# Kernel tuning notes

Hardware: AMD Instinct MI355X
Metric: run time of the kernel (lower is better)

Reference implementation:

```python
import jax, jax.numpy as jnp
import numpy as np

N, D, H, C, E = 16384, 768, 768, 2, 20

def setup_inputs() -> dict:
    key = jax.random.key(0)
    k1, k2, k3, k4, k5, k6 = jax.random.split(key, 6)
    return {
        "embeddings": jax.random.normal(k1, (N, D), dtype=jnp.float32),
        "component_idx": jax.random.randint(k2, (N,), 0, E, dtype=jnp.int64),
        "W1": jax.random.normal(k3, (E, D, H), dtype=jnp.float32) * (1.0 / np.sqrt(D)),
        "b1": jnp.zeros((E, H), dtype=jnp.float32),
        "W2": jax.random.normal(k4, (E, H, C), dtype=jnp.float32) * (1.0 / np.sqrt(H)),
        "b2": jnp.zeros((E, C), dtype=jnp.float32),
    }

def reference(embeddings, component_idx, W1, b1, W2, b2):
    # Each token n goes through expert component_idx[n]:
    #   y = relu(x @ W1[e] + b1[e]) @ W2[e] + b2[e]
    # The torch module's mask/cat/argsort reassembly is mathematically a
    # per-token select of its own expert's output at the original position.
    # Dense-expert formulation (standard jax MoE fallback), then gather.
    h = jax.nn.relu(jnp.einsum('nd,edh->enh', embeddings, W1) + b1[:, None, :])  # [E,N,H]
    y = jnp.einsum('enh,ehc->enc', h, W2) + b2[:, None, :]                        # [E,N,C]
    n_idx = jnp.arange(embeddings.shape[0])
    return y[component_idx, n_idx]  # [N,C]
```

## Files before the change

### kernel.cpp

```cpp
#include <hip/hip_runtime.h>

#define N_D 768
#define N_H 768
#define N_C 2
#define N_E 20
#define MT 128
#define NT 128
#define BK 32
#define KT (N_D / BK)
#define MAX_TILES 160
#define NCOL (N_H / NT)
#define ROWB (N_D * 2)
#define W1BLKS (N_E * (N_D / 64) * (N_H / 64))

typedef __attribute__((ext_vector_type(8))) short short8;
typedef __attribute__((ext_vector_type(4))) float f32x4;

__device__ __forceinline__ unsigned short f2bf(float f) {
  unsigned u = __builtin_bit_cast(unsigned, f);
  u += 0x7FFFu + ((u >> 16) & 1u);
  return (unsigned short)(u >> 16);
}

#define GLD_LDS16(gp, lp)                                                        \
  __builtin_amdgcn_global_load_lds(                                              \
      (const __attribute__((address_space(1))) void*)(gp),                       \
      (__attribute__((address_space(3))) void*)(lp), 16, 0, 0)


__global__ __launch_bounds__(256) void k_prep(const float* __restrict__ W1,
                                              unsigned short* __restrict__ W1t,
                                              const int* __restrict__ cidx,
                                              int* __restrict__ counts, int n,
                                              int hb) {
  __shared__ float tile[64][65];
  __shared__ int lc[N_E];
  if ((int)blockIdx.x < W1BLKS) {
    int bid = blockIdx.x;
    int e = bid / 144;
    int rem = bid - e * 144;
    int h0 = (rem % 12) * 64, d0 = (rem / 12) * 64;
    const float* src = W1 + (size_t)e * N_D * N_H;
    unsigned short* dst = W1t + (size_t)e * N_H * N_D;
    int tx = threadIdx.x & 15, ty = threadIdx.x >> 4;
#pragma unroll
    for (int s = 0; s < 4; ++s) {
      int d = s * 16 + ty;
      float4 v = *(const float4*)&src[(size_t)(d0 + d) * N_H + h0 + tx * 4];
      tile[d][tx * 4 + 0] = v.x;
      tile[d][tx * 4 + 1] = v.y;
      tile[d][tx * 4 + 2] = v.z;
      tile[d][tx * 4 + 3] = v.w;
    }
    __syncthreads();
    int px = threadIdx.x & 7, py = threadIdx.x >> 3;
#pragma unroll
    for (int s = 0; s < 2; ++s) {
      int h = s * 32 + py;
      short8 v;
#pragma unroll
      for (int j = 0; j < 8; ++j)
        v[j] = (short)f2bf(tile[px * 8 + j][h]);
      *(short8*)&dst[(size_t)(h0 + h) * N_D + d0 + px * 8] = v;
    }
  } else {
    int b = blockIdx.x - W1BLKS;
    if (threadIdx.x < N_E) lc[threadIdx.x] = 0;
    __syncthreads();
    for (int i = b * 256 + threadIdx.x; i < n; i += hb * 256) {
      int e = cidx[i];
      e = e < 0 ? 0 : (e >= N_E ? N_E - 1 : e);
      atomicAdd(&lc[e], 1);
    }
    __syncthreads();
    if (threadIdx.x < N_E) atomicAdd(&counts[threadIdx.x], lc[threadIdx.x]);
  }
}


__global__ void k_scan(const int* __restrict__ counts, int* __restrict__ offsets,
                       int* __restrict__ cursor, int* __restrict__ tiles,
                       int* __restrict__ numTiles) {
  int lane = threadIdx.x;
  int c = (lane < N_E) ? counts[lane] : 0;
  int nt = (c + MT - 1) / MT;
  int cs = c, ts = nt;
#pragma unroll
  for (int s = 1; s < 32; s <<= 1) {
    int t1 = __shfl_up(cs, s, 64);
    int t2 = __shfl_up(ts, s, 64);
    if (lane >= s) {
      cs += t1;
      ts += t2;
    }
  }
  int coff = cs - c;
  int tbase = ts - nt;
  if (lane < N_E) {
    offsets[lane] = coff;
    cursor[lane] = coff;
    for (int m = 0; m < nt; ++m) {
      int t = tbase + m;
      if (t < MAX_TILES) tiles[t] = (lane << 8) | m;
    }
  }
  if (lane == N_E - 1) *numTiles = ts > MAX_TILES ? MAX_TILES : ts;
}


#define SG_TOK 64

__global__ __launch_bounds__(256) void k_scatter_gather(
    const int* __restrict__ cidx, int* __restrict__ cursor,
    int* __restrict__ sorted, const float* __restrict__ emb,
    unsigned short* __restrict__ Xg, int n) {
  __shared__ int lc[N_E];
  __shared__ int lbase[N_E];
  __shared__ int pos_s[SG_TOK];
  const int tid = threadIdx.x;
  const int nb = (n + SG_TOK - 1) / SG_TOK;
  if ((int)blockIdx.x >= nb) {
    ushort4 z = {0, 0, 0, 0};
    ushort4* dst = (ushort4*)(Xg + (size_t)n * N_D);
    for (int k = tid; k < MT * N_D / 4; k += 256) dst[k] = z;
    return;
  }
  const int base_tok = blockIdx.x * SG_TOK;
  if (tid < N_E) lc[tid] = 0;
  __syncthreads();
  const int i = base_tok + tid;
  int e = 0, p = 0;
  if (tid < SG_TOK && i < n) {
    e = cidx[i];
    e = e < 0 ? 0 : (e >= N_E ? N_E - 1 : e);
    p = atomicAdd(&lc[e], 1);
  }
  __syncthreads();
  if (tid < N_E) lbase[tid] = atomicAdd(&cursor[tid], lc[tid]);
  __syncthreads();
  if (tid < SG_TOK) {
    if (i < n) {
      int pos = lbase[e] + p;
      sorted[pos] = i;
      pos_s[tid] = pos;
    } else {
      pos_s[tid] = -1;
    }
  }
  __syncthreads();
  const int wid = tid >> 6, lane = tid & 63;
  int nrows = n - base_tok;
  if (nrows > SG_TOK) nrows = SG_TOK;
  for (int rr = wid; rr < nrows; rr += 4) {
    const float4* s = (const float4*)(emb + (size_t)(base_tok + rr) * N_D);
    ushort4* d = (ushort4*)(Xg + (size_t)pos_s[rr] * N_D);
#pragma unroll
    for (int p2 = 0; p2 < 3; ++p2) {
      float4 v = s[lane + p2 * 64];
      ushort4 o;
      o.x = f2bf(v.x);
      o.y = f2bf(v.y);
      o.z = f2bf(v.z);
      o.w = f2bf(v.w);
      d[lane + p2 * 64] = o;
    }
  }
}


__global__ __launch_bounds__(256, 4) void k_gemm(
    const unsigned short* __restrict__ Xg, const unsigned short* __restrict__ W1t,
    const float* __restrict__ b1, const float* __restrict__ W2,
    const float* __restrict__ b2, const int* __restrict__ sorted,
    const int* __restrict__ counts, const int* __restrict__ offsets,
    const int* __restrict__ tiles, const int* __restrict__ numTiles,
    float* __restrict__ out) {
  const int nactive = *numTiles * NCOL;
  const int lin = (int)blockIdx.y * NCOL + (int)blockIdx.x;
  if (lin >= nactive) return;
  const int q = nactive >> 3, r = nactive & 7;
  const int c = lin & 7, ii = lin >> 3;
  const int wgid = (c < r ? c * (q + 1) : r * (q + 1) + (c - r) * q) + ii;
  const int tileIdx = wgid / NCOL;
  const int n0 = (wgid - tileIdx * NCOL) * NT;

  const int tv = tiles[tileIdx];
  const int e = tv >> 8;
  const int m0 = (tv & 255) * MT;
  const int off = offsets[e];
  const int cnt_rel = counts[e] - m0;

  __shared__ unsigned short lA[2][MT * BK];
  __shared__ unsigned short lB[2][NT * BK];

  const int tid = threadIdx.x;
  const int wid = tid >> 6, lane = tid & 63;
  const int wm = (wid >> 1) * 64, wn = (wid & 1) * 64;
  const int quad = lane >> 4, lm = lane & 15;

  const int R0 = wid * 32 + lm;
  const char* agp = (const char*)Xg + (size_t)(off + m0 + R0) * ROWB + quad * 16;
  const char* bgp = (const char*)W1t + (size_t)e * N_H * ROWB +
                    (size_t)(n0 + R0) * ROWB + quad * 16;
  unsigned short* lap[2] = {&lA[0][(wid * 32) * BK], &lA[1][(wid * 32) * BK]};
  unsigned short* lbp[2] = {&lB[0][(wid * 32) * BK], &lB[1][(wid * 32) * BK]};

#define ISSUE_BATCH(kk, b)                                                       \
  do {                                                                           \
    const char* a_ = agp + (kk)*64;                                              \
    const char* b_ = bgp + (kk)*64;                                              \
    GLD_LDS16(a_, lap[b]);                                                       \
    GLD_LDS16(a_ + 16 * ROWB, lap[b] + 16 * BK);                                 \
    GLD_LDS16(b_, lbp[b]);                                                       \
    GLD_LDS16(b_ + 16 * ROWB, lbp[b] + 16 * BK);                                 \
  } while (0)

  f32x4 acc[4][4] = {};

  ISSUE_BATCH(0, 0);
  ISSUE_BATCH(1, 1);

  const int fa = quad * 128 + lm * 8;

  for (int kt = 0; kt < KT; ++kt) {
    const int cur = kt & 1;
    asm volatile("s_waitcnt vmcnt(4)\n\ts_barrier" ::: "memory");
    short8 af[4], bfr[4];
    for (int i = 0; i < 4; ++i)
      af[i] = *(const short8*)&lA[cur][((wm >> 4) + i) * 512 + fa];
    for (int j = 0; j < 4; ++j)
      bfr[j] = *(const short8*)&lB[cur][((wn >> 4) + j) * 512 + fa];
    asm volatile("s_waitcnt lgkmcnt(0)\n\ts_barrier" ::: "memory");
    int kk = kt + 2;
    if (kk >= KT) kk -= KT;
    ISSUE_BATCH(kk, cur);
    for (int i = 0; i < 4; ++i)
      for (int j = 0; j < 4; ++j)
        acc[i][j] =
            __builtin_amdgcn_mfma_f32_16x16x32_bf16(af[i], bfr[j], acc[i][j], 0, 0, 0);
  }

  float y0[4][4], y1[4][4];
  for (int i = 0; i < 4; ++i)
    for (int r2 = 0; r2 < 4; ++r2) y0[i][r2] = y1[i][r2] = 0.f;

  for (int j = 0; j < 4; ++j) {
    int col = n0 + wn + j * 16 + lm;
    float bias = b1[e * N_H + col];
    float2 w2 = *(const float2*)&W2[((size_t)e * N_H + col) * N_C];
    for (int i = 0; i < 4; ++i) {
      f32x4 a = acc[i][j];
      for (int r2 = 0; r2 < 4; ++r2) {
        float h = a[r2] + bias;
        h = h > 0.f ? h : 0.f;
        y0[i][r2] += h * w2.x;
        y1[i][r2] += h * w2.y;
      }
    }
  }
  for (int s = 1; s < 16; s <<= 1) {
    for (int i = 0; i < 4; ++i)
      for (int r2 = 0; r2 < 4; ++r2) {
        y0[i][r2] += __shfl_xor(y0[i][r2], s, 64);
        y1[i][r2] += __shfl_xor(y1[i][r2], s, 64);
      }
  }
  if (lm == 0) {
    const bool add_bias = (n0 == 0) && (wn == 0);
    float bb0 = add_bias ? b2[e * N_C + 0] : 0.f;
    float bb1 = add_bias ? b2[e * N_C + 1] : 0.f;
    for (int i = 0; i < 4; ++i) {
      for (int r2 = 0; r2 < 4; ++r2) {
        int mrel = wm + i * 16 + quad * 4 + r2;
        if (mrel < cnt_rel) {
          int token = sorted[off + m0 + mrel];
          atomicAdd(&out[(size_t)token * N_C + 0], y0[i][r2] + bb0);
          atomicAdd(&out[(size_t)token * N_C + 1], y1[i][r2] + bb1);
        }
      }
    }
  }
}


extern "C" void kernel_launch(void* const* d_in, const int* in_sizes, int n_in,
                              void* d_out, int out_size, void* d_ws, size_t ws_size,
                              hipStream_t stream) {
  const float* emb = (const float*)d_in[0];
  const int* cidx = (const int*)d_in[1];
  const float* W1 = (const float*)d_in[2];
  const float* b1 = (const float*)d_in[3];
  const float* W2 = (const float*)d_in[4];
  const float* b2 = (const float*)d_in[5];
  float* out = (float*)d_out;
  const int n = in_sizes[1];

  char* ws = (char*)d_ws;
  int* counts = (int*)ws;
  int* offsets = (int*)(ws + 128);
  int* cursor = (int*)(ws + 256);
  int* numTiles = (int*)(ws + 384);
  int* tiles = (int*)(ws + 512);
  int* sorted = (int*)(ws + 2048);
  size_t sorted_bytes = ((size_t)n * 4 + 255) & ~(size_t)255;
  unsigned short* Xg = (unsigned short*)(ws + 2048 + sorted_bytes);
  int pcap = n + MT;
  unsigned short* W1t = Xg + (size_t)pcap * N_D;

  hipMemsetAsync(d_ws, 0, 2048, stream);
  hipMemsetAsync(d_out, 0, (size_t)out_size * sizeof(float), stream);
  int hb = (n + 255) / 256;
  k_prep<<<W1BLKS + hb, 256, 0, stream>>>(W1, W1t, cidx, counts, n, hb);
  k_scan<<<1, 64, 0, stream>>>(counts, offsets, cursor, tiles, numTiles);
  int nb64 = (n + SG_TOK - 1) / SG_TOK;
  k_scatter_gather<<<nb64 + 1, 256, 0, stream>>>(cidx, cursor, sorted, emb, Xg, n);
  k_gemm<<<dim3(NCOL, MAX_TILES), 256, 0, stream>>>(
      Xg, W1t, b1, W2, b2, sorted, counts, offsets, tiles, numTiles, out);
}
```

Before: 221.8 us.

## Fold memsets into prep kernel, use per-block count partials, retune launch bounds

Both hipMemsetAsync calls are removed. The histogram blocks in k_prep now write per-block count partials, which k_scan sums, so the workspace no longer needs zeroing. Those same histogram blocks also zero the output buffer. Separately, the scatter/gather kernel moves to 512-thread blocks, and the GEMM's launch-bounds occupancy hint drops from 4 to 2, allowing more registers per thread at the cost of fewer resident waves.

```diff
diff --git a/kernel.cpp b/kernel.cpp
--- a/kernel.cpp
+++ b/kernel.cpp
@@ -12,6 +12,7 @@
 #define NCOL (N_H / NT)
 #define ROWB (N_D * 2)
 #define W1BLKS (N_E * (N_D / 64) * (N_H / 64))
+#define HB 64
 
 typedef __attribute__((ext_vector_type(8))) short short8;
 typedef __attribute__((ext_vector_type(4))) float f32x4;
@@ -31,8 +32,8 @@
 __global__ __launch_bounds__(256) void k_prep(const float* __restrict__ W1,
                                               unsigned short* __restrict__ W1t,
                                               const int* __restrict__ cidx,
-                                              int* __restrict__ counts, int n,
-                                              int hb) {
+                                              int* __restrict__ partials,
+                                              float* __restrict__ out, int n) {
   __shared__ float tile[64][65];
   __shared__ int lc[N_E];
   if ((int)blockIdx.x < W1BLKS) {
@@ -65,24 +66,30 @@
     }
   } else {
     int b = blockIdx.x - W1BLKS;
-    if (threadIdx.x < N_E) lc[threadIdx.x] = 0;
+    int tid = threadIdx.x;
+    if (tid < N_E) lc[tid] = 0;
     __syncthreads();
-    for (int i = b * 256 + threadIdx.x; i < n; i += hb * 256) {
+    for (int i = b * 256 + tid; i < n; i += HB * 256) {
       int e = cidx[i];
       e = e < 0 ? 0 : (e >= N_E ? N_E - 1 : e);
       atomicAdd(&lc[e], 1);
     }
     __syncthreads();
-    if (threadIdx.x < N_E) atomicAdd(&counts[threadIdx.x], lc[threadIdx.x]);
-  }
-}
-
-
-__global__ void k_scan(const int* __restrict__ counts, int* __restrict__ offsets,
-                       int* __restrict__ cursor, int* __restrict__ tiles,
-                       int* __restrict__ numTiles) {
+    if (tid < N_E) partials[b * 32 + tid] = lc[tid];
+    for (int idx = b * 256 + tid; idx < N_C * n; idx += HB * 256) out[idx] = 0.f;
+  }
+}
+
+
+__global__ void k_scan(const int* __restrict__ partials, int* __restrict__ counts,
+                       int* __restrict__ offsets, int* __restrict__ cursor,
+                       int* __restrict__ tiles, int* __restrict__ numTiles) {
   int lane = threadIdx.x;
-  int c = (lane < N_E) ? counts[lane] : 0;
+  int c = 0;
+  if (lane < N_E) {
+#pragma unroll
+    for (int b = 0; b < HB; ++b) c += partials[b * 32 + lane];
+  }
   int nt = (c + MT - 1) / MT;
   int cs = c, ts = nt;
 #pragma unroll
@@ -97,6 +104,7 @@
   int coff = cs - c;
   int tbase = ts - nt;
   if (lane < N_E) {
+    counts[lane] = c;
     offsets[lane] = coff;
     cursor[lane] = coff;
     for (int m = 0; m < nt; ++m) {
@@ -110,7 +118,7 @@
 
 #define SG_TOK 64
 
-__global__ __launch_bounds__(256) void k_scatter_gather(
+__global__ __launch_bounds__(512) void k_scatter_gather(
     const int* __restrict__ cidx, int* __restrict__ cursor,
     int* __restrict__ sorted, const float* __restrict__ emb,
     unsigned short* __restrict__ Xg, int n) {
@@ -122,7 +130,7 @@
   if ((int)blockIdx.x >= nb) {
     ushort4 z = {0, 0, 0, 0};
     ushort4* dst = (ushort4*)(Xg + (size_t)n * N_D);
-    for (int k = tid; k < MT * N_D / 4; k += 256) dst[k] = z;
+    for (int k = tid; k < MT * N_D / 4; k += 512) dst[k] = z;
     return;
   }
   const int base_tok = blockIdx.x * SG_TOK;
@@ -151,7 +159,7 @@
   const int wid = tid >> 6, lane = tid & 63;
   int nrows = n - base_tok;
   if (nrows > SG_TOK) nrows = SG_TOK;
-  for (int rr = wid; rr < nrows; rr += 4) {
+  for (int rr = wid; rr < nrows; rr += 8) {
     const float4* s = (const float4*)(emb + (size_t)(base_tok + rr) * N_D);
     ushort4* d = (ushort4*)(Xg + (size_t)pos_s[rr] * N_D);
 #pragma unroll
@@ -168,7 +176,7 @@
 }
 
 
-__global__ __launch_bounds__(256, 4) void k_gemm(
+__global__ __launch_bounds__(256, 2) void k_gemm(
     const unsigned short* __restrict__ Xg, const unsigned short* __restrict__ W1t,
     const float* __restrict__ b1, const float* __restrict__ W2,
     const float* __restrict__ b2, const int* __restrict__ sorted,
@@ -301,19 +309,17 @@
   int* cursor = (int*)(ws + 256);
   int* numTiles = (int*)(ws + 384);
   int* tiles = (int*)(ws + 512);
-  int* sorted = (int*)(ws + 2048);
+  int* partials = (int*)(ws + 2048);
+  int* sorted = (int*)(ws + 2048 + HB * 32 * 4);
   size_t sorted_bytes = ((size_t)n * 4 + 255) & ~(size_t)255;
-  unsigned short* Xg = (unsigned short*)(ws + 2048 + sorted_bytes);
+  unsigned short* Xg = (unsigned short*)(ws + 2048 + HB * 32 * 4 + sorted_bytes);
   int pcap = n + MT;
   unsigned short* W1t = Xg + (size_t)pcap * N_D;
 
-  hipMemsetAsync(d_ws, 0, 2048, stream);
-  hipMemsetAsync(d_out, 0, (size_t)out_size * sizeof(float), stream);
-  int hb = (n + 255) / 256;
-  k_prep<<<W1BLKS + hb, 256, 0, stream>>>(W1, W1t, cidx, counts, n, hb);
-  k_scan<<<1, 64, 0, stream>>>(counts, offsets, cursor, tiles, numTiles);
+  k_prep<<<W1BLKS + HB, 256, 0, stream>>>(W1, W1t, cidx, partials, out, n);
+  k_scan<<<1, 64, 0, stream>>>(partials, counts, offsets, cursor, tiles, numTiles);
   int nb64 = (n + SG_TOK - 1) / SG_TOK;
-  k_scatter_gather<<<nb64 + 1, 256, 0, stream>>>(cidx, cursor, sorted, emb, Xg, n);
+  k_scatter_gather<<<nb64 + 1, 512, 0, stream>>>(cidx, cursor, sorted, emb, Xg, n);
   k_gemm<<<dim3(NCOL, MAX_TILES), 256, 0, stream>>>(
       Xg, W1t, b1, W2, b2, sorted, counts, offsets, tiles, numTiles, out);
 }
```

Result: faster. 207.3 us (-6.5%).

## Merge histogram and scan into one kernel, fuse W1 transpose with scatter-gather

Applied to the files above, without the earlier changes.

Expert counting and the prefix scan now run in a single one-block kernel, which also removes both memsets: counts are written directly and the output zeroing moves into the padding block of the mid kernel. The W1 bf16 transpose blocks are folded into the scatter-gather launch with an XCD-aware block mapping, so the weight conversion overlaps with the embedding gather. This goes from five stream operations to three. The gemm launch bound drops from 4 to 2 waves per SIMD, allowing more registers per thread. The cost is a serial single-block histogram over all 16K tokens.

```diff
diff --git a/kernel.cpp b/kernel.cpp
--- a/kernel.cpp
+++ b/kernel.cpp
@@ -12,6 +12,7 @@
 #define NCOL (N_H / NT)
 #define ROWB (N_D * 2)
 #define W1BLKS (N_E * (N_D / 64) * (N_H / 64))
+#define SG_TOK 64
 
 typedef __attribute__((ext_vector_type(8))) short short8;
 typedef __attribute__((ext_vector_type(4))) float f32x4;
@@ -28,21 +29,90 @@
       (__attribute__((address_space(3))) void*)(lp), 16, 0, 0)
 
 
-__global__ __launch_bounds__(256) void k_prep(const float* __restrict__ W1,
-                                              unsigned short* __restrict__ W1t,
-                                              const int* __restrict__ cidx,
-                                              int* __restrict__ counts, int n,
-                                              int hb) {
+__global__ __launch_bounds__(256) void k_front(const int* __restrict__ cidx,
+                                               int* __restrict__ counts,
+                                               int* __restrict__ offsets,
+                                               int* __restrict__ cursor,
+                                               int* __restrict__ tiles,
+                                               int* __restrict__ numTiles, int n) {
+  __shared__ int lc[4][N_E];
+  __shared__ int tot[N_E];
+  const int tid = threadIdx.x;
+  const int w = tid >> 6;
+  for (int k = tid; k < 4 * N_E; k += 256) ((int*)lc)[k] = 0;
+  __syncthreads();
+  const int4* c4 = (const int4*)cidx;
+  const int nv = n >> 2;
+  for (int i = tid; i < nv; i += 256) {
+    int4 v = c4[i];
+    int e0 = v.x < 0 ? 0 : (v.x >= N_E ? N_E - 1 : v.x);
+    int e1 = v.y < 0 ? 0 : (v.y >= N_E ? N_E - 1 : v.y);
+    int e2 = v.z < 0 ? 0 : (v.z >= N_E ? N_E - 1 : v.z);
+    int e3 = v.w < 0 ? 0 : (v.w >= N_E ? N_E - 1 : v.w);
+    atomicAdd(&lc[w][e0], 1);
+    atomicAdd(&lc[w][e1], 1);
+    atomicAdd(&lc[w][e2], 1);
+    atomicAdd(&lc[w][e3], 1);
+  }
+  for (int i = (nv << 2) + tid; i < n; i += 256) {
+    int e = cidx[i];
+    e = e < 0 ? 0 : (e >= N_E ? N_E - 1 : e);
+    atomicAdd(&lc[w][e], 1);
+  }
+  __syncthreads();
+  if (tid < N_E) tot[tid] = lc[0][tid] + lc[1][tid] + lc[2][tid] + lc[3][tid];
+  __syncthreads();
+  if (tid < 64) {
+    int lane = tid;
+    int c = (lane < N_E) ? tot[lane] : 0;
+    int nt = (c + MT - 1) / MT;
+    int cs = c, ts = nt;
+#pragma unroll
+    for (int s = 1; s < 32; s <<= 1) {
+      int t1 = __shfl_up(cs, s, 64);
+      int t2 = __shfl_up(ts, s, 64);
+      if (lane >= s) {
+        cs += t1;
+        ts += t2;
+      }
+    }
+    int coff = cs - c;
+    int tbase = ts - nt;
+    if (lane < N_E) {
+      counts[lane] = c;
+      offsets[lane] = coff;
+      cursor[lane] = coff;
+      for (int m = 0; m < nt; ++m) {
+        int t = tbase + m;
+        if (t < MAX_TILES) tiles[t] = (lane << 8) | m;
+      }
+    }
+    if (lane == N_E - 1) *numTiles = ts > MAX_TILES ? MAX_TILES : ts;
+  }
+}
+
+
+__global__ __launch_bounds__(256) void k_mid(
+    const int* __restrict__ cidx, int* __restrict__ cursor,
+    int* __restrict__ sorted, const float* __restrict__ emb,
+    unsigned short* __restrict__ Xg, const float* __restrict__ W1,
+    unsigned short* __restrict__ W1t, float* __restrict__ out, int n, int nbsg) {
   __shared__ float tile[64][65];
   __shared__ int lc[N_E];
-  if ((int)blockIdx.x < W1BLKS) {
-    int bid = blockIdx.x;
-    int e = bid / 144;
-    int rem = bid - e * 144;
+  __shared__ int lbase[N_E];
+  __shared__ int pos_s[SG_TOK];
+  const int tid = threadIdx.x;
+
+  if ((int)blockIdx.x >= nbsg) {
+    int w1i = blockIdx.x - nbsg;
+    int xcd = w1i & 7, ii = w1i >> 3;
+    int wgid = xcd * (W1BLKS / 8) + ii;
+    int e = wgid / 144;
+    int rem = wgid - e * 144;
     int h0 = (rem % 12) * 64, d0 = (rem / 12) * 64;
     const float* src = W1 + (size_t)e * N_D * N_H;
     unsigned short* dst = W1t + (size_t)e * N_H * N_D;
-    int tx = threadIdx.x & 15, ty = threadIdx.x >> 4;
+    int tx = tid & 15, ty = tid >> 4;
 #pragma unroll
     for (int s = 0; s < 4; ++s) {
       int d = s * 16 + ty;
@@ -53,7 +123,7 @@
       tile[d][tx * 4 + 3] = v.w;
     }
     __syncthreads();
-    int px = threadIdx.x & 7, py = threadIdx.x >> 3;
+    int px = tid & 7, py = tid >> 3;
 #pragma unroll
     for (int s = 0; s < 2; ++s) {
       int h = s * 32 + py;
@@ -63,66 +133,17 @@
         v[j] = (short)f2bf(tile[px * 8 + j][h]);
       *(short8*)&dst[(size_t)(h0 + h) * N_D + d0 + px * 8] = v;
     }
-  } else {
-    int b = blockIdx.x - W1BLKS;
-    if (threadIdx.x < N_E) lc[threadIdx.x] = 0;
-    __syncthreads();
-    for (int i = b * 256 + threadIdx.x; i < n; i += hb * 256) {
-      int e = cidx[i];
-      e = e < 0 ? 0 : (e >= N_E ? N_E - 1 : e);
-      atomicAdd(&lc[e], 1);
-    }
-    __syncthreads();
-    if (threadIdx.x < N_E) atomicAdd(&counts[threadIdx.x], lc[threadIdx.x]);
-  }
-}
-
-
-__global__ void k_scan(const int* __restrict__ counts, int* __restrict__ offsets,
-                       int* __restrict__ cursor, int* __restrict__ tiles,
-                       int* __restrict__ numTiles) {
-  int lane = threadIdx.x;
-  int c = (lane < N_E) ? counts[lane] : 0;
-  int nt = (c + MT - 1) / MT;
-  int cs = c, ts = nt;
-#pragma unroll
-  for (int s = 1; s < 32; s <<= 1) {
-    int t1 = __shfl_up(cs, s, 64);
-    int t2 = __shfl_up(ts, s, 64);
-    if (lane >= s) {
-      cs += t1;
-      ts += t2;
-    }
-  }
-  int coff = cs - c;
-  int tbase = ts - nt;
-  if (lane < N_E) {
-    offsets[lane] = coff;
-    cursor[lane] = coff;
-    for (int m = 0; m < nt; ++m) {
-      int t = tbase + m;
-      if (t < MAX_TILES) tiles[t] = (lane << 8) | m;
-    }
-  }
-  if (lane == N_E - 1) *numTiles = ts > MAX_TILES ? MAX_TILES : ts;
-}
-
-
-#define SG_TOK 64
-
-__global__ __launch_bounds__(256) void k_scatter_gather(
-    const int* __restrict__ cidx, int* __restrict__ cursor,
-    int* __restrict__ sorted, const float* __restrict__ emb,
-    unsigned short* __restrict__ Xg, int n) {
-  __shared__ int lc[N_E];
-  __shared__ int lbase[N_E];
-  __shared__ int pos_s[SG_TOK];
-  const int tid = threadIdx.x;
+    return;
+  }
+
   const int nb = (n + SG_TOK - 1) / SG_TOK;
   if ((int)blockIdx.x >= nb) {
     ushort4 z = {0, 0, 0, 0};
     ushort4* dst = (ushort4*)(Xg + (size_t)n * N_D);
     for (int k = tid; k < MT * N_D / 4; k += 256) dst[k] = z;
+    float4 zf = {0.f, 0.f, 0.f, 0.f};
+    float4* of = (float4*)out;
+    for (int k = tid; k < N_C * n / 4; k += 256) of[k] = zf;
     return;
   }
   const int base_tok = blockIdx.x * SG_TOK;
@@ -168,7 +189,7 @@
 }
 
 
-__global__ __launch_bounds__(256, 4) void k_gemm(
+__global__ __launch_bounds__(256, 2) void k_gemm(
     const unsigned short* __restrict__ Xg, const unsigned short* __restrict__ W1t,
     const float* __restrict__ b1, const float* __restrict__ W2,
     const float* __restrict__ b2, const int* __restrict__ sorted,
@@ -307,13 +328,10 @@
   int pcap = n + MT;
   unsigned short* W1t = Xg + (size_t)pcap * N_D;
 
-  hipMemsetAsync(d_ws, 0, 2048, stream);
-  hipMemsetAsync(d_out, 0, (size_t)out_size * sizeof(float), stream);
-  int hb = (n + 255) / 256;
-  k_prep<<<W1BLKS + hb, 256, 0, stream>>>(W1, W1t, cidx, counts, n, hb);
-  k_scan<<<1, 64, 0, stream>>>(counts, offsets, cursor, tiles, numTiles);
-  int nb64 = (n + SG_TOK - 1) / SG_TOK;
-  k_scatter_gather<<<nb64 + 1, 256, 0, stream>>>(cidx, cursor, sorted, emb, Xg, n);
+  k_front<<<1, 256, 0, stream>>>(cidx, counts, offsets, cursor, tiles, numTiles, n);
+  int nbsg = (n + SG_TOK - 1) / SG_TOK + 1;
+  k_mid<<<nbsg + W1BLKS, 256, 0, stream>>>(cidx, cursor, sorted, emb, Xg, W1, W1t,
+                                           out, n, nbsg);
   k_gemm<<<dim3(NCOL, MAX_TILES), 256, 0, stream>>>(
       Xg, W1t, b1, W2, b2, sorted, counts, offsets, tiles, numTiles, out);
 }
```

Measured after the change: 205.9 us. 7.2% less time.
